# Optimization experiments

Hardware: AMD Instinct MI355X
Metric: run time of the kernel (lower is better)

The kernel has to match this reference:

```python
import math
import jax, jax.numpy as jnp
import numpy as np

NUM_ANGLE = 8
NUM_RADIAL = 3
RADIAL_MIN = 0.08
RADIAL_MAX = 0.9
EPS = 1e-6


def _hann(n):
    # torch.hann_window(n, periodic=False)
    return 0.5 * (1.0 - jnp.cos(2.0 * jnp.pi * jnp.arange(n, dtype=jnp.float32) / (n - 1)))


def _to_luma(img):
    # img: [B, 3, H, W] -> [B, H, W]
    return 0.2989 * img[:, 0] + 0.587 * img[:, 1] + 0.114 * img[:, 2]


def _log_magnitude(img):
    x = _to_luma(img).astype(jnp.float32)  # [B, H, W]
    H, W = x.shape[-2], x.shape[-1]
    win = _hann(H)[:, None] * _hann(W)[None, :]  # [H, W]
    x = x * win
    spec = jnp.fft.fftshift(jnp.fft.fft2(x, axes=(-2, -1)), axes=(-2, -1))
    return jnp.log1p(jnp.abs(spec))  # [B, H, W]


def _polar_masks(H, W):
    y = jnp.linspace(-1.0, 1.0, H, dtype=jnp.float32)
    x = jnp.linspace(-1.0, 1.0, W, dtype=jnp.float32)
    yy, xx = jnp.meshgrid(y, x, indexing='ij')
    radius = jnp.sqrt(xx * xx + yy * yy)
    radius = radius / jnp.maximum(radius.max(), EPS)
    angle = jnp.remainder(jnp.arctan2(yy, xx), math.pi)

    r_edges = jnp.linspace(RADIAL_MIN, RADIAL_MAX, NUM_RADIAL + 1, dtype=jnp.float32)
    a_edges = jnp.linspace(0.0, math.pi, NUM_ANGLE + 1, dtype=jnp.float32)

    r0 = r_edges[:-1][:, None, None]
    r1 = r_edges[1:][:, None, None]
    rmask = (radius[None] >= r0) & (radius[None] < r1)           # [R, H, W]
    rmask = rmask.at[-1].set((radius >= r_edges[-2]) & (radius <= r_edges[-1]))

    t0 = a_edges[:-1][:, None, None]
    t1 = a_edges[1:][:, None, None]
    amask = (angle[None] >= t0) & (angle[None] < t1)             # [A, H, W]
    amask = amask.at[-1].set((angle >= a_edges[-2]) & (angle <= a_edges[-1]))

    return (rmask[:, None] & amask[None, :]).astype(jnp.float32)  # [R, A, H, W]


def _sector_energies(img):
    mag = _log_magnitude(img)                          # [B, H, W]
    masks = _polar_masks(mag.shape[-2], mag.shape[-1])  # [R, A, H, W]
    mask_sum = jnp.maximum(masks.sum(axis=(-2, -1)), EPS)        # [R, A]
    masked_sum = jnp.einsum('bhw,rahw->bra', mag, masks)         # [B, R, A]
    energies = masked_sum / mask_sum[None]
    energies = energies / jnp.maximum(energies.sum(axis=-1, keepdims=True), EPS)
    return energies


def setup_inputs() -> dict:
    key = jax.random.key(0)
    k1, k2 = jax.random.split(key)
    B, C, H, W = 16, 3, 512, 512
    prediction = jax.random.uniform(k1, (B, C, H, W), dtype=jnp.float32)
    target = jax.random.uniform(k2, (B, C, H, W), dtype=jnp.float32)
    radial_weights = jnp.array([0.5, 1.0, 1.2], dtype=jnp.float32).reshape(1, NUM_RADIAL, 1)
    return {"prediction": prediction, "target": target, "radial_weights": radial_weights}


def reference(prediction, target, radial_weights):
    pred_e = _sector_energies(prediction)   # [B, R, A]
    tgt_e = _sector_energies(target)
    diff = pred_e - tgt_e
    dist = jnp.sqrt(diff * diff + EPS)      # charbonnier
    return (dist * radial_weights).mean()
```

## Files before the change

kernel.cpp:

```cpp
#include <hip/hip_runtime.h>
#include <math.h>

#define PI_F 3.14159265358979323846f
#define TWO_PI_F 6.28318530717958647692f
#define RSQ2 0.70710678118654752440f

#define LGKM(n) __asm__ volatile("s_waitcnt lgkmcnt(" #n ")" ::: "memory")
#define LADDR(a) ((a) + ((a) >> 3))

__device__ __forceinline__ float2 cadd(float2 a, float2 b){ return make_float2(a.x+b.x, a.y+b.y); }
__device__ __forceinline__ float2 csub(float2 a, float2 b){ return make_float2(a.x-b.x, a.y-b.y); }
__device__ __forceinline__ float2 cmul(float2 a, float2 b){ return make_float2(a.x*b.x - a.y*b.y, a.x*b.y + a.y*b.x); }
__device__ __forceinline__ float2 cw1(float2 a){ return make_float2(RSQ2*(a.x+a.y), RSQ2*(a.y-a.x)); }
__device__ __forceinline__ float2 cw2(float2 a){ return make_float2(a.y, -a.x); }
__device__ __forceinline__ float2 cw3(float2 a){ return make_float2(RSQ2*(a.y-a.x), -RSQ2*(a.x+a.y)); }

__device__ __forceinline__ void dft8(float2* v){
    float2 a0=cadd(v[0],v[4]), a1=cadd(v[1],v[5]), a2=cadd(v[2],v[6]), a3=cadd(v[3],v[7]);
    float2 b0=csub(v[0],v[4]);
    float2 b1=cw1(csub(v[1],v[5]));
    float2 b2=cw2(csub(v[2],v[6]));
    float2 b3=cw3(csub(v[3],v[7]));
    float2 c0=cadd(a0,a2), c2=csub(a0,a2), c1=cadd(a1,a3), c3=cw2(csub(a1,a3));
    float2 d0=cadd(b0,b2), d2=csub(b0,b2), d1=cadd(b1,b3), d3=cw2(csub(b1,b3));
    v[0]=cadd(c0,c1); v[1]=csub(c0,c1);
    v[2]=cadd(c2,c3); v[3]=csub(c2,c3);
    v[4]=cadd(d0,d1); v[5]=csub(d0,d1);
    v[6]=cadd(d2,d3); v[7]=csub(d2,d3);
}

__device__ __forceinline__ void calc_pows(float2 w, float2* p){
    p[0] = w;
    p[1] = cmul(w, w);
    p[2] = cmul(p[1], w);
    p[3] = cmul(p[1], p[1]);
    p[4] = cmul(p[2], p[1]);
    p[5] = cmul(p[2], p[2]);
    p[6] = cmul(p[3], p[2]);
}

__device__ __forceinline__ void stage_store(float2* wl, const float2* v, const float2* p,
                                            int base, int step){
    constexpr int br[8] = {0,4,2,6,1,5,3,7};
    wl[LADDR(base)] = v[0];
    #pragma unroll
    for (int c = 1; c < 8; ++c) wl[LADDR(base + step*c)] = cmul(v[br[c]], p[c-1]);
}

__device__ __forceinline__ void stage_load(const float2* wl, float2* v, int j){
    #pragma unroll
    for (int i = 0; i < 8; ++i) v[i] = wl[LADDR(j + 64*i)];
}

__device__ __forceinline__ void fft512_pair(float2* va, float2* vb,
                                            float2* wlA, float2* wlB,
                                            float2 tw0, float2 tw1, int j){
    float2 pw[7];
    calc_pows(tw0, pw);
    dft8(va);
    dft8(vb);
    stage_store(wlA, va, pw, 8 * j, 1);
    stage_store(wlB, vb, pw, 8 * j, 1);
    LGKM(8);
    stage_load(wlA, va, j);
    LGKM(8);
    stage_load(wlB, vb, j);
    LGKM(8);
    calc_pows(tw1, pw);
    dft8(va);
    stage_store(wlA, va, pw, (j & 7) + 64 * (j >> 3), 8);
    LGKM(8);
    dft8(vb);
    stage_store(wlB, vb, pw, (j & 7) + 64 * (j >> 3), 8);
    LGKM(8);
    stage_load(wlA, va, j);
    LGKM(8);
    stage_load(wlB, vb, j);
    LGKM(8);
    dft8(va);
    LGKM(0);
    dft8(vb);
}

__device__ __forceinline__ int sector_id(int hm, int wm) {
    const float step = 2.0f / 511.0f;
    float y = -1.0f + step * (float)hm;
    float x = -1.0f + step * (float)wm;
    float radius = sqrtf(x * x + y * y);
    float r = radius / sqrtf(2.0f);
    float a = atan2f(y, x);
    a = fmodf(a, PI_F);
    if (a < 0.0f) a += PI_F;

    const float rstep = (0.9f - 0.08f) / 3.0f;
    const float re0 = 0.08f;
    const float re1 = 0.08f + rstep;
    const float re2 = 0.08f + 2.0f * rstep;
    const float re3 = 0.9f;
    int rb;
    if      (r >= re0 && r < re1)  rb = 0;
    else if (r >= re1 && r < re2)  rb = 1;
    else if (r >= re2 && r <= re3) rb = 2;
    else return -1;

    const float astep = PI_F / 8.0f;
    int ab = 7;
    #pragma unroll
    for (int i = 0; i < 7; ++i) {
        float t0 = astep * (float)i;
        float t1 = astep * (float)(i + 1);
        if (a >= t0 && a < t1) { ab = i; break; }
    }
    return rb * 8 + ab;
}

__device__ __forceinline__ float hannf(int i) {
    return 0.5f * (1.0f - __cosf(TWO_PI_F * (float)i / 511.0f));
}

__device__ __forceinline__ float lumaf(const float* b, size_t off){
    return 0.2989f*b[off] + 0.587f*b[off+262144] + 0.114f*b[off+524288];
}

__device__ __forceinline__ void write_row(float4* __restrict__ out4, size_t kbase, int hp,
                                          const float2* v, int partner, int j){
    constexpr int br[8] = {0,4,2,6,1,5,3,7};
    #pragma unroll
    for (int c = 0; c < 4; ++c) {
        int k = j + 64 * c;
        float2 zk = v[br[c]];
        float mx = __shfl(v[br[7 - c]].x, partner, 64);
        float my = __shfl(v[br[7 - c]].y, partner, 64);
        float2 zs = v[br[(8 - c) & 7]];
        float2 zm = make_float2(j == 0 ? zs.x : mx, j == 0 ? zs.y : my);
        float4 o = make_float4(0.5f*(zk.x+zm.x), 0.5f*(zk.y-zm.y),
                               0.5f*(zk.y+zm.y), 0.5f*(zm.x-zk.x));
        if (k != 0) out4[(kbase + (size_t)k) * 256 + hp] = o;
    }
    if (j == 0) {
        float2 z0 = v[br[0]], z4 = v[br[4]];
        out4[kbase * 256 + hp] = make_float4(z0.x, z4.x, z0.y, z4.y);
    }
}

__device__ __forceinline__ void bin_col(const float2* v,
                                        const unsigned char* __restrict__ mw1,
                                        const unsigned char* __restrict__ mw2,
                                        float* wb, int rep, int j){
    constexpr int br[8] = {0,4,2,6,1,5,3,7};
    #pragma unroll
    for (int c = 0; c < 8; ++c) {
        float2 z = v[br[c]];
        float mag = __logf(1.0f + sqrtf(z.x * z.x + z.y * z.y));
        int hm = j + 64 * ((c + 4) & 7);
        int s1 = mw1[hm]; if (s1 < 24) atomicAdd(&wb[rep + s1], mag);
        int hm2 = (256 - (j + 64 * c)) & 511;
        int s2 = mw2[hm2]; if (s2 < 24) atomicAdd(&wb[rep + s2], mag);
    }
}

__global__ __launch_bounds__(256, 4) void rowfft_kernel(const float* __restrict__ pred,
                                                        const float* __restrict__ tgt,
                                                        float4* __restrict__ out4,
                                                        unsigned char* __restrict__ mapT,
                                                        unsigned short* __restrict__ cnt_u16,
                                                        float* __restrict__ acc_rep) {
    __shared__ float2 lds[4 * 1152];
    __shared__ float cbins[24];
    int blk = blockIdx.x;
    int img = blk >> 4;
    int pb  = blk & 15;
    int t = threadIdx.x;
    int wv = t >> 6, j = t & 63;
    int hp0 = pb * 16 + wv * 4;
    int h0 = 2 * hp0;
    float2* wlA = lds + wv * 1152;
    float2* wlB = wlA + 576;

    if (blk < 48) acc_rep[blk * 256 + t] = 0.0f;
    if (t < 24) cbins[t] = 0.0f;
    __syncthreads();
    #pragma unroll
    for (int mi = 0; mi < 2; ++mi) {
        int idx = blk * 512 + mi * 256 + t;
        int wm = idx >> 9, hm = idx & 511;
        int s = sector_id(hm, wm);
        mapT[idx] = (unsigned char)(s < 0 ? 255 : s);
        if (s >= 0) atomicAdd(&cbins[s], 1.0f);
    }

    const float* base = (img < 16) ? (pred + (size_t)img * 786432)
                                   : (tgt  + (size_t)(img - 16) * 786432);
    float wh[8];
    #pragma unroll
    for (int r = 0; r < 8; ++r) wh[r] = hannf(h0 + r);
    float2 va[8], vb[8], vc[8], vd[8];
    #pragma unroll
    for (int i = 0; i < 8; ++i) {
        int w = j + 64 * i;
        float ww = hannf(w);
        size_t off = (size_t)h0 * 512 + w;
        float l0 = lumaf(base, off);
        float l1 = lumaf(base, off + 512);
        float l2 = lumaf(base, off + 1024);
        float l3 = lumaf(base, off + 1536);
        float l4 = lumaf(base, off + 2048);
        float l5 = lumaf(base, off + 2560);
        float l6 = lumaf(base, off + 3072);
        float l7 = lumaf(base, off + 3584);
        va[i] = make_float2(l0 * (wh[0] * ww), l1 * (wh[1] * ww));
        vb[i] = make_float2(l2 * (wh[2] * ww), l3 * (wh[3] * ww));
        vc[i] = make_float2(l4 * (wh[4] * ww), l5 * (wh[5] * ww));
        vd[i] = make_float2(l6 * (wh[6] * ww), l7 * (wh[7] * ww));
    }

    float sn, cs;
    __sincosf(-TWO_PI_F * (float)j / 512.0f, &sn, &cs);
    float2 tw0 = make_float2(cs, sn);
    __sincosf(-TWO_PI_F * (float)((j >> 3) << 3) / 512.0f, &sn, &cs);
    float2 tw1 = make_float2(cs, sn);

    fft512_pair(va, vb, wlA, wlB, tw0, tw1, j);
    fft512_pair(vc, vd, wlA, wlB, tw0, tw1, j);

    size_t kbase = (size_t)img * 256;
    int partner = (64 - j) & 63;
    write_row(out4, kbase, hp0 + 0, va, partner, j);
    write_row(out4, kbase, hp0 + 1, vb, partner, j);
    write_row(out4, kbase, hp0 + 2, vc, partner, j);
    write_row(out4, kbase, hp0 + 3, vd, partner, j);

    __syncthreads();
    if (t < 24) cnt_u16[t * 512 + blk] = (unsigned short)(int)cbins[t];
}

__global__ __launch_bounds__(256, 4) void colfft_kernel(const float2* __restrict__ buf,
                                                        const unsigned char* __restrict__ mapT,
                                                        float* __restrict__ acc_rep) {
    __shared__ float2 lds[4 * 1152];
    int blk = blockIdx.x;
    int t = threadIdx.x;
    int wv = t >> 6, j = t & 63;
    int qg = blk * 4 + wv;
    int img = qg >> 6;
    int q = qg & 63;
    int w0 = 4 * q;
    float2* wlA = lds + wv * 1152;
    float2* wlB = wlA + 576;

    const float2* col = buf + (size_t)(img * 256 + w0) * 512;
    float2 va[8], vb[8], vc[8], vd[8];
    #pragma unroll
    for (int i = 0; i < 8; ++i) va[i] = col[j + 64 * i];
    #pragma unroll
    for (int i = 0; i < 8; ++i) vb[i] = col[512 + j + 64 * i];
    #pragma unroll
    for (int i = 0; i < 8; ++i) vc[i] = col[1024 + j + 64 * i];
    #pragma unroll
    for (int i = 0; i < 8; ++i) vd[i] = col[1536 + j + 64 * i];

    float sn, cs;
    __sincosf(-TWO_PI_F * (float)j / 512.0f, &sn, &cs);
    float2 tw0 = make_float2(cs, sn);
    __sincosf(-TWO_PI_F * (float)((j >> 3) << 3) / 512.0f, &sn, &cs);
    float2 tw1 = make_float2(cs, sn);

    fft512_pair(va, vb, wlA, wlB, tw0, tw1, j);
    fft512_pair(vc, vd, wlA, wlB, tw0, tw1, j);

    float* wb = (float*)wlA;
    #pragma unroll
    for (int i = 0; i < 4; ++i) { int ii = j + 64 * i; if (ii < 200) wb[ii] = 0.0f; }
    LGKM(0);

    constexpr int br[8] = {0,4,2,6,1,5,3,7};
    int rep = (j & 7) * 25;
    bool pairw = (qg == 0);
    if (pairw) {
        int partner = (64 - j) & 63;
        const unsigned char* mwA1 = mapT + (size_t)256 * 512;
        const unsigned char* mwA2 = mapT;
        #pragma unroll
        for (int c = 0; c < 8; ++c) {
            float2 zk = va[br[c]];
            float mx = __shfl(va[br[7 - c]].x, partner, 64);
            float my = __shfl(va[br[7 - c]].y, partner, 64);
            float2 zs = va[br[(8 - c) & 7]];
            float2 zm = make_float2(j == 0 ? zs.x : mx, j == 0 ? zs.y : my);
            float f0x = 0.5f*(zk.x+zm.x), f0y = 0.5f*(zk.y-zm.y);
            float f1x = 0.5f*(zk.y+zm.y), f1y = 0.5f*(zm.x-zk.x);
            float mag0 = __logf(1.0f + sqrtf(f0x*f0x + f0y*f0y));
            float mag1 = __logf(1.0f + sqrtf(f1x*f1x + f1y*f1y));
            int hm = j + 64 * ((c + 4) & 7);
            int s1 = mwA1[hm]; if (s1 < 24) atomicAdd(&wb[rep + s1], mag0);
            int s2 = mwA2[hm]; if (s2 < 24) atomicAdd(&wb[rep + s2], mag1);
        }
    } else {
        int wA = w0;
        bin_col(va, mapT + (size_t)((wA + 256) & 511) * 512,
                    mapT + (size_t)((256 - wA) & 511) * 512, wb, rep, j);
    }
    {
        int w = w0 + 1;
        bin_col(vb, mapT + (size_t)((w + 256) & 511) * 512,
                    mapT + (size_t)((256 - w) & 511) * 512, wb, rep, j);
        w = w0 + 2;
        bin_col(vc, mapT + (size_t)((w + 256) & 511) * 512,
                    mapT + (size_t)((256 - w) & 511) * 512, wb, rep, j);
        w = w0 + 3;
        bin_col(vd, mapT + (size_t)((w + 256) & 511) * 512,
                    mapT + (size_t)((256 - w) & 511) * 512, wb, rep, j);
    }
    LGKM(0);
    if (j < 24) {
        float sum = 0.0f;
        #pragma unroll
        for (int r = 0; r < 8; ++r) sum += wb[r * 25 + j];
        atomicAdd(&acc_rep[(qg & 15) * 768 + img * 24 + j], sum);
    }
}

__global__ __launch_bounds__(256) void final_kernel(const float* __restrict__ acc_rep,
                                                    const unsigned short* __restrict__ cnt_u16,
                                                    const float* __restrict__ rw,
                                                    float* __restrict__ out) {
    __shared__ float accs[768];
    __shared__ float cnts[24];
    __shared__ float ep[384], et[384], red[384];
    int t = threadIdx.x;
    for (int o = t; o < 768; o += 256) {
        float s = 0.0f;
        #pragma unroll
        for (int r = 0; r < 16; ++r) s += acc_rep[r * 768 + o];
        accs[o] = s;
    }
    if (t < 192) {
        int s = t >> 3, g = t & 7;
        const ushort4* p = (const ushort4*)(cnt_u16 + s * 512 + g * 64);
        float sum = 0.0f;
        #pragma unroll
        for (int i = 0; i < 16; ++i) { ushort4 u = p[i]; sum += (float)(u.x + u.y + u.z + u.w); }
        sum += __shfl_down(sum, 4, 8);
        sum += __shfl_down(sum, 2, 8);
        sum += __shfl_down(sum, 1, 8);
        if (g == 0) cnts[s] = sum;
    }
    __syncthreads();
    for (int idx = t; idx < 384; idx += 256) {
        int b = idx / 24, s = idx - b * 24;
        float cnt = fmaxf(cnts[s], 1e-6f);
        ep[idx] = accs[b * 24 + s] / cnt;
        et[idx] = accs[(16 + b) * 24 + s] / cnt;
    }
    __syncthreads();
    for (int idx = t; idx < 384; idx += 256) {
        int b = idx / 24, s = idx - b * 24, r = s >> 3;
        int gbase = b * 24 + r * 8;
        float sp = 0.0f, st = 0.0f;
        #pragma unroll
        for (int a = 0; a < 8; ++a) { sp += ep[gbase + a]; st += et[gbase + a]; }
        float pe = ep[idx] / fmaxf(sp, 1e-6f);
        float te = et[idx] / fmaxf(st, 1e-6f);
        float d = pe - te;
        red[idx] = sqrtf(d * d + 1e-6f) * rw[r];
    }
    __syncthreads();
    if (t < 128) red[t] += red[t + 128] + red[t + 256];
    __syncthreads();
    if (t < 64) {
        float vv = red[t] + red[t + 64];
        #pragma unroll
        for (int o = 32; o > 0; o >>= 1) vv += __shfl_down(vv, o, 64);
        if (t == 0) out[0] = vv / 384.0f;
    }
}

extern "C" void kernel_launch(void* const* d_in, const int* in_sizes, int n_in,
                              void* d_out, int out_size, void* d_ws, size_t ws_size,
                              hipStream_t stream) {
    const float* pred = (const float*)d_in[0];
    const float* tgt  = (const float*)d_in[1];
    const float* rw   = (const float*)d_in[2];

    char* ws = (char*)d_ws;
    float* acc_rep       = (float*)ws;
    unsigned short* cnt  = (unsigned short*)(ws + 49152);
    unsigned char* mapT  = (unsigned char*)(ws + 98304);
    float2* buf          = (float2*)(ws + 360448);

    rowfft_kernel<<<512, 256, 0, stream>>>(pred, tgt, (float4*)buf, mapT, cnt, acc_rep);
    colfft_kernel<<<512, 256, 0, stream>>>(buf, mapT, acc_rep);
    final_kernel<<<1, 256, 0, stream>>>(acc_rep, cnt, rw, (float*)d_out);
}
```

Measured before the change: 209.8 us.

## Store row-FFT output row-major and double row-kernel grid with fewer rows per wave

The row FFT kernel now writes its half-spectrum output row-major (contiguous per row pair) rather than transposed, and each wave processes two row pairs instead of four, doubling the grid to 1024 blocks. The column FFT kernel then gathers each column from row-major float4 data, picking the even or odd half of each packed pair. Per-block sector-count storage and the final reduction are widened to match. This makes the row kernel's stores coalesced and gives it more parallelism, but the column kernel's loads become strided across rows, and the per-block mask/count work is spread over more blocks.

```diff
diff --git a/kernel.cpp b/kernel.cpp
--- a/kernel.cpp
+++ b/kernel.cpp
@@ -122,9 +122,10 @@
     return 0.2989f*b[off] + 0.587f*b[off+262144] + 0.114f*b[off+524288];
 }
 
-__device__ __forceinline__ void write_row(float4* __restrict__ out4, size_t kbase, int hp,
-                                          const float2* v, int partner, int j){
+__device__ __forceinline__ void write_row_T(float4* __restrict__ out4, size_t ibase, int hp,
+                                            const float2* v, int partner, int j){
     constexpr int br[8] = {0,4,2,6,1,5,3,7};
+    float4* row = out4 + (ibase + (size_t)hp) * 256;
     #pragma unroll
     for (int c = 0; c < 4; ++c) {
         int k = j + 64 * c;
@@ -135,11 +136,11 @@
         float2 zm = make_float2(j == 0 ? zs.x : mx, j == 0 ? zs.y : my);
         float4 o = make_float4(0.5f*(zk.x+zm.x), 0.5f*(zk.y-zm.y),
                                0.5f*(zk.y+zm.y), 0.5f*(zm.x-zk.x));
-        if (k != 0) out4[(kbase + (size_t)k) * 256 + hp] = o;
+        if (k != 0) row[k] = o;
     }
     if (j == 0) {
         float2 z0 = v[br[0]], z4 = v[br[4]];
-        out4[kbase * 256 + hp] = make_float4(z0.x, z4.x, z0.y, z4.y);
+        row[0] = make_float4(z0.x, z4.x, z0.y, z4.y);
     }
 }
 
@@ -168,21 +169,21 @@
     __shared__ float2 lds[4 * 1152];
     __shared__ float cbins[24];
     int blk = blockIdx.x;
-    int img = blk >> 4;
-    int pb  = blk & 15;
+    int img = blk >> 5;
+    int pb  = blk & 31;
     int t = threadIdx.x;
     int wv = t >> 6, j = t & 63;
-    int hp0 = pb * 16 + wv * 4;
-    int h0 = 2 * hp0;
+    int hpA = pb * 8 + wv * 2;
+    int hpB = hpA + 1;
+    int h0 = 2 * hpA;
     float2* wlA = lds + wv * 1152;
     float2* wlB = wlA + 576;
 
     if (blk < 48) acc_rep[blk * 256 + t] = 0.0f;
     if (t < 24) cbins[t] = 0.0f;
     __syncthreads();
-    #pragma unroll
-    for (int mi = 0; mi < 2; ++mi) {
-        int idx = blk * 512 + mi * 256 + t;
+    {
+        int idx = blk * 256 + t;
         int wm = idx >> 9, hm = idx & 511;
         int s = sector_id(hm, wm);
         mapT[idx] = (unsigned char)(s < 0 ? 255 : s);
@@ -191,27 +192,20 @@
 
     const float* base = (img < 16) ? (pred + (size_t)img * 786432)
                                    : (tgt  + (size_t)(img - 16) * 786432);
-    float wh[8];
-    #pragma unroll
-    for (int r = 0; r < 8; ++r) wh[r] = hannf(h0 + r);
-    float2 va[8], vb[8], vc[8], vd[8];
+    float whA0 = hannf(h0), whA1 = hannf(h0 + 1);
+    float whB0 = hannf(h0 + 2), whB1 = hannf(h0 + 3);
+    float2 va[8], vb[8];
     #pragma unroll
     for (int i = 0; i < 8; ++i) {
         int w = j + 64 * i;
         float ww = hannf(w);
-        size_t off = (size_t)h0 * 512 + w;
-        float l0 = lumaf(base, off);
-        float l1 = lumaf(base, off + 512);
-        float l2 = lumaf(base, off + 1024);
-        float l3 = lumaf(base, off + 1536);
-        float l4 = lumaf(base, off + 2048);
-        float l5 = lumaf(base, off + 2560);
-        float l6 = lumaf(base, off + 3072);
-        float l7 = lumaf(base, off + 3584);
-        va[i] = make_float2(l0 * (wh[0] * ww), l1 * (wh[1] * ww));
-        vb[i] = make_float2(l2 * (wh[2] * ww), l3 * (wh[3] * ww));
-        vc[i] = make_float2(l4 * (wh[4] * ww), l5 * (wh[5] * ww));
-        vd[i] = make_float2(l6 * (wh[6] * ww), l7 * (wh[7] * ww));
+        size_t off0 = (size_t)h0 * 512 + w;
+        float l0 = lumaf(base, off0);
+        float l1 = lumaf(base, off0 + 512);
+        float l2 = lumaf(base, off0 + 1024);
+        float l3 = lumaf(base, off0 + 1536);
+        va[i] = make_float2(l0 * (whA0 * ww), l1 * (whA1 * ww));
+        vb[i] = make_float2(l2 * (whB0 * ww), l3 * (whB1 * ww));
     }
 
     float sn, cs;
@@ -221,20 +215,17 @@
     float2 tw1 = make_float2(cs, sn);
 
     fft512_pair(va, vb, wlA, wlB, tw0, tw1, j);
-    fft512_pair(vc, vd, wlA, wlB, tw0, tw1, j);
-
-    size_t kbase = (size_t)img * 256;
+
+    size_t ibase = (size_t)img * 256;
     int partner = (64 - j) & 63;
-    write_row(out4, kbase, hp0 + 0, va, partner, j);
-    write_row(out4, kbase, hp0 + 1, vb, partner, j);
-    write_row(out4, kbase, hp0 + 2, vc, partner, j);
-    write_row(out4, kbase, hp0 + 3, vd, partner, j);
-
-    __syncthreads();
-    if (t < 24) cnt_u16[t * 512 + blk] = (unsigned short)(int)cbins[t];
-}
-
-__global__ __launch_bounds__(256, 4) void colfft_kernel(const float2* __restrict__ buf,
+    write_row_T(out4, ibase, hpA, va, partner, j);
+    write_row_T(out4, ibase, hpB, vb, partner, j);
+
+    __syncthreads();
+    if (t < 24) cnt_u16[t * 1024 + blk] = (unsigned short)(int)cbins[t];
+}
+
+__global__ __launch_bounds__(256, 4) void colfft_kernel(const float4* __restrict__ buf4,
                                                         const unsigned char* __restrict__ mapT,
                                                         float* __restrict__ acc_rep) {
     __shared__ float2 lds[4 * 1152];
@@ -248,16 +239,19 @@
     float2* wlA = lds + wv * 1152;
     float2* wlB = wlA + 576;
 
-    const float2* col = buf + (size_t)(img * 256 + w0) * 512;
+    const float4* b4 = buf4 + ((size_t)img * 256) * 256 + w0;
     float2 va[8], vb[8], vc[8], vd[8];
     #pragma unroll
-    for (int i = 0; i < 8; ++i) va[i] = col[j + 64 * i];
-    #pragma unroll
-    for (int i = 0; i < 8; ++i) vb[i] = col[512 + j + 64 * i];
-    #pragma unroll
-    for (int i = 0; i < 8; ++i) vc[i] = col[1024 + j + 64 * i];
-    #pragma unroll
-    for (int i = 0; i < 8; ++i) vd[i] = col[1536 + j + 64 * i];
+    for (int i = 0; i < 8; ++i) {
+        int h = j + 64 * i;
+        const float4* row = b4 + (size_t)(h >> 1) * 256;
+        float4 q0 = row[0], q1 = row[1], q2 = row[2], q3 = row[3];
+        bool odd = (h & 1) != 0;
+        va[i] = odd ? make_float2(q0.z, q0.w) : make_float2(q0.x, q0.y);
+        vb[i] = odd ? make_float2(q1.z, q1.w) : make_float2(q1.x, q1.y);
+        vc[i] = odd ? make_float2(q2.z, q2.w) : make_float2(q2.x, q2.y);
+        vd[i] = odd ? make_float2(q3.z, q3.w) : make_float2(q3.x, q3.y);
+    }
 
     float sn, cs;
     __sincosf(-TWO_PI_F * (float)j / 512.0f, &sn, &cs);
@@ -336,10 +330,10 @@
     }
     if (t < 192) {
         int s = t >> 3, g = t & 7;
-        const ushort4* p = (const ushort4*)(cnt_u16 + s * 512 + g * 64);
+        const ushort4* p = (const ushort4*)(cnt_u16 + s * 1024 + g * 128);
         float sum = 0.0f;
         #pragma unroll
-        for (int i = 0; i < 16; ++i) { ushort4 u = p[i]; sum += (float)(u.x + u.y + u.z + u.w); }
+        for (int i = 0; i < 32; ++i) { ushort4 u = p[i]; sum += (float)(u.x + u.y + u.z + u.w); }
         sum += __shfl_down(sum, 4, 8);
         sum += __shfl_down(sum, 2, 8);
         sum += __shfl_down(sum, 1, 8);
@@ -386,9 +380,9 @@
     float* acc_rep       = (float*)ws;
     unsigned short* cnt  = (unsigned short*)(ws + 49152);
     unsigned char* mapT  = (unsigned char*)(ws + 98304);
-    float2* buf          = (float2*)(ws + 360448);
-
-    rowfft_kernel<<<512, 256, 0, stream>>>(pred, tgt, (float4*)buf, mapT, cnt, acc_rep);
-    colfft_kernel<<<512, 256, 0, stream>>>(buf, mapT, acc_rep);
+    float4* buf4         = (float4*)(ws + 360448);
+
+    rowfft_kernel<<<1024, 256, 0, stream>>>(pred, tgt, buf4, mapT, cnt, acc_rep);
+    colfft_kernel<<<512, 256, 0, stream>>>(buf4, mapT, acc_rep);
     final_kernel<<<1, 256, 0, stream>>>(acc_rep, cnt, rw, (float*)d_out);
 }
```

After: 189.5 us. -9.7%, faster.
